# Optimization experiments

Measured on AMD Instinct MI355X. Metric: run time of the kernel, lower is better.

## Reference

```python
import jax, jax.numpy as jnp
import numpy as np

D_MODEL = 2048
N_OCTAVES = 3
MIN_BANDWIDTH = 0.25
MIN_CUTOFF = int(D_MODEL * MIN_BANDWIDTH)


def _build_index_maps():
    """Replicates MatryoshkaHarmonicMixing._build_index_maps (static, numpy)."""
    maps = []
    for octave in range(1, N_OCTAVES + 1):
        stride = 2 ** octave
        i = np.arange(MIN_CUTOFF)
        tgt = i * stride
        mask = (tgt < D_MODEL) & (tgt >= MIN_CUTOFF)
        src_idx = i[mask]
        tgt_idx = tgt[mask]
        if src_idx.size:
            maps.append((jnp.asarray(src_idx, dtype=jnp.int32),
                         jnp.asarray(tgt_idx, dtype=jnp.int32)))
        else:
            maps.append(None)
    return maps

_INDEX_MAPS = _build_index_maps()


def setup_inputs() -> dict:
    key = jax.random.key(0)
    kx, kw = jax.random.split(key)
    x = jax.random.normal(kx, (4, 4096, D_MODEL), dtype=jnp.float32)
    # torch init is ones(n_octaves)*0.1; use small random values for a nontrivial test
    weights = jax.random.uniform(kw, (N_OCTAVES,), dtype=jnp.float32)
    return {"x": x, "weights": weights}


def reference(x, weights):
    # out = x + sum_octaves sigmoid(w_o) * scatter(x[..., src_o] -> tgt_o)
    out = x
    for octave, m in enumerate(_INDEX_MAPS):
        if m is None:
            continue
        src, tgt = m
        w = jax.nn.sigmoid(weights[octave])
        # targets are unique within an octave (tgt = i*stride is injective),
        # but use .add to match index_add semantics exactly
        out = out.at[..., tgt].add(w * x[..., src])
    return out
```

## Files before the change

### kernel.cpp

```cpp
#include <hip/hip_runtime.h>


#define D_MODEL 2048

typedef float v4f __attribute__((ext_vector_type(4)));

__global__ __launch_bounds__(256) void mhm_kernel(
    const float* __restrict__ x,
    const float* __restrict__ w,
    float* __restrict__ out)
{
    const float s1 = 1.0f / (1.0f + expf(-w[0]));
    const float s2 = 1.0f / (1.0f + expf(-w[1]));
    const float s3 = 1.0f / (1.0f + expf(-w[2]));

    const long long i = (long long)blockIdx.x * blockDim.x + threadIdx.x;
    const long long e0 = i << 2;
    const int d0 = (int)(e0 & (D_MODEL - 1));
    const long long row = e0 - d0;

    v4f v = reinterpret_cast<const v4f*>(x)[i];

    if (d0 >= 512) {
        if (d0 < 1024) {
            const float2 p = *reinterpret_cast<const float2*>(&x[row + (d0 >> 1)]);
            v.x += s1 * p.x;
            v.z += s1 * p.y;
        }
        v.x += s2 * x[row + (d0 >> 2)];
        if ((d0 & 7) == 0) {
            v.x += s3 * x[row + (d0 >> 3)];
        }
    }

    __builtin_nontemporal_store(v, reinterpret_cast<v4f*>(out) + i);
}

extern "C" void kernel_launch(void* const* d_in, const int* in_sizes, int n_in,
                              void* d_out, int out_size, void* d_ws, size_t ws_size,
                              hipStream_t stream) {
    const float* x = (const float*)d_in[0];
    const float* w = (const float*)d_in[1];
    float* out = (float*)d_out;

    const long long n = (long long)out_size;
    const long long n4 = n >> 2;
    const int threads = 256;
    const int blocks = (int)((n4 + threads - 1) / threads);

    mhm_kernel<<<blocks, threads, 0, stream>>>(x, w, out);
}
```

Baseline: 48.07 us.

## Stage row prefix in LDS and serve harmonic gathers from shared memory

The kernel now runs one 256-thread block per row, with each thread handling two float4 chunks. Threads stage the source range of the row (elements 64..511) into LDS, and after a __syncthreads all strided harmonic gathers read from LDS instead of issuing extra scattered global loads. This cuts redundant global and L2 gather traffic and the divergent load instructions. In exchange it adds a block barrier and halves the grid size.

```diff
diff --git a/kernel.cpp b/kernel.cpp
--- a/kernel.cpp
+++ b/kernel.cpp
@@ -10,30 +10,37 @@
     const float* __restrict__ w,
     float* __restrict__ out)
 {
+    __shared__ float lds[512];
+
     const float s1 = 1.0f / (1.0f + expf(-w[0]));
     const float s2 = 1.0f / (1.0f + expf(-w[1]));
     const float s3 = 1.0f / (1.0f + expf(-w[2]));
 
-    const long long i = (long long)blockIdx.x * blockDim.x + threadIdx.x;
-    const long long e0 = i << 2;
-    const int d0 = (int)(e0 & (D_MODEL - 1));
-    const long long row = e0 - d0;
+    const int t = threadIdx.x;
+    const long long row4 = (long long)blockIdx.x * (D_MODEL / 4);
+    const v4f* __restrict__ x4 = reinterpret_cast<const v4f*>(x);
+    v4f* __restrict__ o4 = reinterpret_cast<v4f*>(out);
 
-    v4f v = reinterpret_cast<const v4f*>(x)[i];
+    v4f a = x4[row4 + t];
+    v4f b = x4[row4 + 256 + t];
 
-    if (d0 >= 512) {
-        if (d0 < 1024) {
-            const float2 p = *reinterpret_cast<const float2*>(&x[row + (d0 >> 1)]);
-            v.x += s1 * p.x;
-            v.z += s1 * p.y;
-        }
-        v.x += s2 * x[row + (d0 >> 2)];
-        if ((d0 & 7) == 0) {
-            v.x += s3 * x[row + (d0 >> 3)];
-        }
+    if (t >= 16 && t < 128) {
+        reinterpret_cast<v4f*>(lds)[t] = a;
     }
+    __syncthreads();
 
-    __builtin_nontemporal_store(v, reinterpret_cast<v4f*>(out) + i);
+    if (t >= 128) {
+        const float2 p = *reinterpret_cast<const float2*>(&lds[t << 1]);
+        a.x += s1 * p.x;
+        a.z += s1 * p.y;
+        a.x += s2 * lds[t];
+        if ((t & 1) == 0) a.x += s3 * lds[t >> 1];
+    }
+    __builtin_nontemporal_store(a, &o4[row4 + t]);
+
+    b.x += s2 * lds[256 + t];
+    if ((t & 1) == 0) b.x += s3 * lds[128 + (t >> 1)];
+    __builtin_nontemporal_store(b, &o4[row4 + 256 + t]);
 }
 
 extern "C" void kernel_launch(void* const* d_in, const int* in_sizes, int n_in,
@@ -43,10 +50,6 @@
     const float* w = (const float*)d_in[1];
     float* out = (float*)d_out;
 
-    const long long n = (long long)out_size;
-    const long long n4 = n >> 2;
-    const int threads = 256;
-    const int blocks = (int)((n4 + threads - 1) / threads);
-
-    mhm_kernel<<<blocks, threads, 0, stream>>>(x, w, out);
+    const int rows = out_size / D_MODEL;
+    mhm_kernel<<<rows, 256, 0, stream>>>(x, w, out);
 }
```

Result: faster. 42.36 us (-11.9%).
